# Kernel optimization log

Measured on AMD Instinct MI355X. Metric: run time of the kernel, lower is better.

## Reference

```python
import jax, jax.numpy as jnp
import numpy as np

WINDOW = 16  # hardcoded in module __init__

B, S, E, H = 2, 2048, 1024, 16
HD = E // H


def setup_inputs() -> dict:
    key = jax.random.key(0)
    k1, k2, k3, k4, k5, k6 = jax.random.split(key, 6)
    input_embeddings = jax.random.normal(k1, (B, S, E), dtype=jnp.float32)
    token_ids = jax.random.randint(k2, (B, S), 0, 32000, dtype=jnp.int64)
    # nn.MultiheadAttention parameters: packed in_proj (3E, E) + bias, out_proj (E, E) + bias
    in_proj_weight = jax.random.normal(k3, (3 * E, E), dtype=jnp.float32) * 0.02
    in_proj_bias = jax.random.normal(k4, (3 * E,), dtype=jnp.float32) * 0.02
    out_proj_weight = jax.random.normal(k5, (E, E), dtype=jnp.float32) * 0.02
    out_proj_bias = jax.random.normal(k6, (E,), dtype=jnp.float32) * 0.02
    return {
        "input_embeddings": input_embeddings,
        "token_ids": token_ids,
        "in_proj_weight": in_proj_weight,
        "in_proj_bias": in_proj_bias,
        "out_proj_weight": out_proj_weight,
        "out_proj_bias": out_proj_bias,
    }


def _blocked_mask(seq_len: int) -> jnp.ndarray:
    # Module sets mask[i, j] = True for j in [i - WINDOW, i] (17 positions).
    # PyTorch bool attn_mask: True = NOT allowed to attend.
    i = jnp.arange(seq_len)[:, None]
    j = jnp.arange(seq_len)[None, :]
    return (j <= i) & (j >= i - WINDOW)  # [S, S] bool, True = masked out


def reference(input_embeddings, token_ids, in_proj_weight, in_proj_bias,
              out_proj_weight, out_proj_bias):
    x = input_embeddings  # [B, S, E]
    b, s, e = x.shape
    # Packed QKV projection (torch Linear: y = x W^T + b)
    qkv = jnp.einsum('bse,fe->bsf', x, in_proj_weight) + in_proj_bias  # [B, S, 3E]
    q, k, v = jnp.split(qkv, 3, axis=-1)
    # Split heads: [B, H, S, HD]
    q = q.reshape(b, s, H, HD).transpose(0, 2, 1, 3)
    k = k.reshape(b, s, H, HD).transpose(0, 2, 1, 3)
    v = v.reshape(b, s, H, HD).transpose(0, 2, 1, 3)
    scale = 1.0 / jnp.sqrt(jnp.asarray(HD, dtype=x.dtype))
    scores = jnp.einsum('bhqd,bhkd->bhqk', q * scale, k)  # [B, H, S, S]
    blocked = _blocked_mask(s)  # True = masked
    scores = jnp.where(blocked[None, None, :, :], -jnp.inf, scores)
    attn = jax.nn.softmax(scores, axis=-1)
    ctx = jnp.einsum('bhqk,bhkd->bhqd', attn, v)  # [B, H, S, HD]
    ctx = ctx.transpose(0, 2, 1, 3).reshape(b, s, e)
    out = jnp.einsum('bse,fe->bsf', ctx, out_proj_weight) + out_proj_bias
    return out
```

## Files before the change

### kernel.cpp

```cpp
#include <hip/hip_runtime.h>

typedef __attribute__((ext_vector_type(8))) __bf16 bf16x8;
typedef __attribute__((ext_vector_type(4))) float f32x4;
typedef unsigned short u16;
typedef unsigned int u32;

#define MFMA16(a, b, c) __builtin_amdgcn_mfma_f32_16x16x32_bf16((a), (b), (c), 0, 0, 0)

__device__ __forceinline__ u16 f2bf(float f) {
  u32 u = __float_as_uint(f);
  return (u16)((u + 0x7fffu + ((u >> 16) & 1u)) >> 16);
}

#define BDIM 2
#define SDIM 2048
#define EDIM 1024
#define HDIM 16
#define HD 64
#define MDIM (BDIM * SDIM)

#define SC_C1 0.1803368801111355f
#define SC_C2 4.328085122667252e+01f

#define SW(r) ((((r) & 3) ^ (((r) >> 2) & 3)))

typedef __attribute__((address_space(3))) void lds_void;
typedef __attribute__((address_space(1))) void g_void;

__device__ __forceinline__ void async_lds16(const void* g, void* lds_byte) {
  __builtin_amdgcn_global_load_lds((const g_void*)g, (lds_void*)lds_byte, 16, 0, 0);
}

__global__ __launch_bounds__(256) void cvt_kernel(const float* __restrict__ src,
                                                  u16* __restrict__ dst, int n) {
  int i = (blockIdx.x * 256 + threadIdx.x) * 8;
  if (i >= n) return;
  float4 f0 = *(const float4*)(src + i);
  float4 f1 = *(const float4*)(src + i + 4);
  union { uint4 u; u16 s[8]; } o;
  o.s[0] = f2bf(f0.x); o.s[1] = f2bf(f0.y); o.s[2] = f2bf(f0.z); o.s[3] = f2bf(f0.w);
  o.s[4] = f2bf(f1.x); o.s[5] = f2bf(f1.y); o.s[6] = f2bf(f1.z); o.s[7] = f2bf(f1.w);
  *(uint4*)(dst + i) = o.u;
}

__global__ __launch_bounds__(256) void gemm_qkv_kernel(
    const u16* __restrict__ X, const u16* __restrict__ W,
    const float* __restrict__ bias, u16* __restrict__ qb,
    u16* __restrict__ kb, u16* __restrict__ vtb) {
  __shared__ __align__(16) u16 As[128 * 32];
  __shared__ __align__(16) u16 Bs[128 * 32];
  const int m0 = blockIdx.x * 128, n0 = blockIdx.y * 128;
  const int t = threadIdx.x;
  const int l = t & 63;
  const int quad = l >> 4, col = l & 15;
  const int wid = t >> 6;
  const int mh = wid & 1, nh = wid >> 1;
  const int wofs = (t & 192) << 4;
  f32x4 acc[4][4] = {};
  const u16* Ab = X + (size_t)m0 * EDIM;
  const u16* Bb = W + (size_t)n0 * EDIM;
  char* AsB = (char*)As;
  char* BsB = (char*)Bs;

  for (int k0 = 0; k0 < EDIM; k0 += 32) {
    __syncthreads();
#pragma unroll
    for (int p = 0; p < 2; p++) {
      int idx = p * 256 + t;
      int row = idx >> 2;
      int kq = (idx & 3) ^ SW(row);
      async_lds16(Ab + (size_t)row * EDIM + k0 + kq * 8, AsB + p * 4096 + wofs);
      async_lds16(Bb + (size_t)row * EDIM + k0 + kq * 8, BsB + p * 4096 + wofs);
    }
    __syncthreads();
    bf16x8 af[4], bfr[4];
#pragma unroll
    for (int i = 0; i < 4; i++) {
      int ra = 64 * mh + 16 * i + col;
      af[i] = *(const bf16x8*)&As[(ra * 4 + (quad ^ SW(ra))) * 8];
      int rb = 64 * nh + 16 * i + col;
      bfr[i] = *(const bf16x8*)&Bs[(rb * 4 + (quad ^ SW(rb))) * 8];
    }
#pragma unroll
    for (int i = 0; i < 4; i++)
#pragma unroll
      for (int j = 0; j < 4; j++)
        acc[i][j] = MFMA16(af[i], bfr[j], acc[i][j]);
  }

#pragma unroll
  for (int i = 0; i < 4; i++)
#pragma unroll
    for (int j = 0; j < 4; j++)
#pragma unroll
      for (int r = 0; r < 4; r++) {
        int m = m0 + 64 * mh + 16 * i + quad * 4 + r;
        int n = n0 + 64 * nh + 16 * j + col;
        float val = acc[i][j][r] + bias[n];
        int which = n >> 10, e = n & 1023;
        int hh = e >> 6, d = e & 63;
        int bb = m >> 11, s = m & 2047;
        u16 bv = f2bf(val);
        size_t hb = (size_t)(bb * HDIM + hh);
        if (which == 0)
          qb[(hb * SDIM + s) * HD + d] = bv;
        else if (which == 1)
          kb[(hb * SDIM + s) * HD + d] = bv;
        else
          vtb[(hb * HD + d) * SDIM + s] = bv;
      }
}

__global__ __launch_bounds__(256) void attn_kernel(
    const u16* __restrict__ qg, const u16* __restrict__ kg,
    const u16* __restrict__ vtg, u16* __restrict__ ctx) {
  __shared__ __align__(16) u16 Ks[64 * 64];
  __shared__ __align__(16) u16 Vs[64 * 64];
  __shared__ __align__(16) u16 Ps[64 * 68];

  const int bh = blockIdx.x;
  const int q0 = blockIdx.y * 64;
  const int t = threadIdx.x;
  const int wid = t >> 6, l = t & 63;
  const int quad = l >> 4, col = l & 15;
  const size_t base = (size_t)bh * SDIM * HD;

  bf16x8 aq[2];
  {
    const u16* qp = qg + base + (size_t)(q0 + 16 * wid + col) * HD + quad * 8;
    aq[0] = *(const bf16x8*)(qp);
    aq[1] = *(const bf16x8*)(qp + 32);
  }
  const int qrow = q0 + 16 * wid + quad * 4;

  const int srow = t >> 3;
  const int g = (t & 7) ^ (srow & 7);
  const u16* kptr = kg + base + (size_t)srow * HD + g * 8;
  const u16* vptr = vtg + base + (size_t)srow * SDIM + g * 8;
  char* ldsK = (char*)Ks + ((t & 192) << 4);
  char* ldsV = (char*)Vs + ((t & 192) << 4);

  float psum[4] = {0.f, 0.f, 0.f, 0.f};
  f32x4 oacc[4] = {};

  for (int kt = 0; kt < SDIM / 64; kt++) {
    const int k0 = kt * 64;
    __syncthreads();
    async_lds16(kptr + (size_t)k0 * HD, ldsK);
    async_lds16(kptr + (size_t)(k0 + 32) * HD, ldsK + 4096);
    async_lds16(vptr + k0, ldsV);
    async_lds16(vptr + (size_t)32 * SDIM + k0, ldsV + 4096);
    __syncthreads();

    f32x4 sc[4] = {};
#pragma unroll
    for (int half = 0; half < 2; half++)
#pragma unroll
      for (int ct = 0; ct < 4; ct++) {
        int r = 16 * ct + col;
        int phys = (4 * half + quad) ^ (r & 7);
        bf16x8 bfrag = *(const bf16x8*)&Ks[r * 64 + phys * 8];
        sc[ct] = MFMA16(aq[half], bfrag, sc[ct]);
      }

    const int pbase = (16 * wid + quad * 4) * 68 + col;
    if (k0 <= q0 + 63 && k0 + 63 >= q0 - 16) {
#pragma unroll
      for (int ct = 0; ct < 4; ct++)
#pragma unroll
        for (int r = 0; r < 4; r++) {
          int i = qrow + r, j = k0 + 16 * ct + col;
          float arg = sc[ct][r] * SC_C1 - SC_C2;
          arg = (j <= i && j + 16 >= i) ? -1.0e30f : arg;
          float p = __builtin_exp2f(arg);
          psum[r] += p;
          Ps[pbase + r * 68 + 16 * ct] = f2bf(p);
        }
    } else {
#pragma unroll
      for (int ct = 0; ct < 4; ct++)
#pragma unroll
        for (int r = 0; r < 4; r++) {
          float p = __builtin_exp2f(sc[ct][r] * SC_C1 - SC_C2);
          psum[r] += p;
          Ps[pbase + r * 68 + 16 * ct] = f2bf(p);
        }
    }

#pragma unroll
    for (int half = 0; half < 2; half++) {
      bf16x8 pa = *(const bf16x8*)&Ps[(16 * wid + col) * 68 + half * 32 + quad * 8];
#pragma unroll
      for (int dt = 0; dt < 4; dt++) {
        int vr = 16 * dt + col;
        int phys = (4 * half + quad) ^ (vr & 7);
        bf16x8 vbf = *(const bf16x8*)&Vs[vr * 64 + phys * 8];
        oacc[dt] = MFMA16(pa, vbf, oacc[dt]);
      }
    }
  }

#pragma unroll
  for (int off = 1; off < 16; off <<= 1)
#pragma unroll
    for (int r = 0; r < 4; r++) psum[r] += __shfl_xor(psum[r], off, 64);

  const int b = bh >> 4, h = bh & 15;
  float linv[4];
#pragma unroll
  for (int r = 0; r < 4; r++) linv[r] = 1.0f / psum[r];
#pragma unroll
  for (int dt = 0; dt < 4; dt++)
#pragma unroll
    for (int r = 0; r < 4; r++) {
      int qgl = qrow + r;
      int d = 16 * dt + col;
      ctx[((size_t)(b * SDIM + qgl)) * EDIM + h * HD + d] =
          f2bf(oacc[dt][r] * linv[r]);
    }
}

__global__ __launch_bounds__(256) void gemm_out_kernel(
    const u16* __restrict__ A, const u16* __restrict__ W,
    const float* __restrict__ bias, float* __restrict__ out) {
  __shared__ __align__(16) u16 As[128 * 32];
  __shared__ __align__(16) u16 Bs[128 * 32];
  const int m0 = blockIdx.x * 128, n0 = blockIdx.y * 128;
  const int t = threadIdx.x;
  const int l = t & 63;
  const int quad = l >> 4, col = l & 15;
  const int wid = t >> 6;
  const int mh = wid & 1, nh = wid >> 1;
  const int wofs = (t & 192) << 4;
  f32x4 acc[4][4] = {};
  const u16* Ab = A + (size_t)m0 * EDIM;
  const u16* Bb = W + (size_t)n0 * EDIM;
  char* AsB = (char*)As;
  char* BsB = (char*)Bs;

  for (int k0 = 0; k0 < EDIM; k0 += 32) {
    __syncthreads();
#pragma unroll
    for (int p = 0; p < 2; p++) {
      int idx = p * 256 + t;
      int row = idx >> 2;
      int kq = (idx & 3) ^ SW(row);
      async_lds16(Ab + (size_t)row * EDIM + k0 + kq * 8, AsB + p * 4096 + wofs);
      async_lds16(Bb + (size_t)row * EDIM + k0 + kq * 8, BsB + p * 4096 + wofs);
    }
    __syncthreads();
    bf16x8 af[4], bfr[4];
#pragma unroll
    for (int i = 0; i < 4; i++) {
      int ra = 64 * mh + 16 * i + col;
      af[i] = *(const bf16x8*)&As[(ra * 4 + (quad ^ SW(ra))) * 8];
      int rb = 64 * nh + 16 * i + col;
      bfr[i] = *(const bf16x8*)&Bs[(rb * 4 + (quad ^ SW(rb))) * 8];
    }
#pragma unroll
    for (int i = 0; i < 4; i++)
#pragma unroll
      for (int j = 0; j < 4; j++)
        acc[i][j] = MFMA16(af[i], bfr[j], acc[i][j]);
  }

#pragma unroll
  for (int i = 0; i < 4; i++)
#pragma unroll
    for (int j = 0; j < 4; j++)
#pragma unroll
      for (int r = 0; r < 4; r++) {
        int m = m0 + 64 * mh + 16 * i + quad * 4 + r;
        int n = n0 + 64 * nh + 16 * j + col;
        out[(size_t)m * EDIM + n] = acc[i][j][r] + bias[n];
      }
}

extern "C" void kernel_launch(void* const* d_in, const int* in_sizes, int n_in,
                              void* d_out, int out_size, void* d_ws,
                              size_t ws_size, hipStream_t stream) {
  const float* x = (const float*)d_in[0];
  const float* in_w = (const float*)d_in[2];
  const float* in_b = (const float*)d_in[3];
  const float* out_w = (const float*)d_in[4];
  const float* out_b = (const float*)d_in[5];
  float* out = (float*)d_out;

  char* ws = (char*)d_ws;
  u16* Xb  = (u16*)ws;
  u16* ctx = (u16*)ws;
  u16* qb  = (u16*)(ws + (size_t)( 8 << 20));
  u16* kb  = (u16*)(ws + (size_t)(16 << 20));
  u16* vtb = (u16*)(ws + (size_t)(24 << 20));
  u16* Wib = (u16*)(ws + (size_t)(32 << 20));
  u16* Wob = (u16*)(ws + (size_t)(38 << 20));

  cvt_kernel<<<2048, 256, 0, stream>>>(x, Xb, MDIM * EDIM);
  cvt_kernel<<<1536, 256, 0, stream>>>(in_w, Wib, 3 * EDIM * EDIM);
  cvt_kernel<<<512, 256, 0, stream>>>(out_w, Wob, EDIM * EDIM);

  gemm_qkv_kernel<<<dim3(MDIM / 128, 3 * EDIM / 128), 256, 0, stream>>>(
      Xb, Wib, in_b, qb, kb, vtb);
  attn_kernel<<<dim3(BDIM * HDIM, SDIM / 64), 256, 0, stream>>>(qb, kb, vtb, ctx);
  gemm_out_kernel<<<dim3(MDIM / 128, EDIM / 128), 256, 0, stream>>>(
      ctx, Wob, out_b, out);
}
```

Baseline: 241.0 us.

## Double attention query tile per block, transpose V GEMM tiles, simplify bf16 rounding

The attention kernel now gives each block 128 query rows (32 per wave, two 16-row subtiles), so every K/V tile loaded into LDS is reused by twice as many queries. This halves global K/V traffic and barrier count, at the cost of more registers and half as many blocks. The QKV GEMM swaps MFMA operands for the V blocks so that the transposed V stores become contiguous along the sequence dimension. The bf16 conversion drops round-to-nearest-even for a plain round-half-up, which saves a few ALU ops but can change rounding on ties.

```diff
diff --git a/kernel.cpp b/kernel.cpp
--- a/kernel.cpp
+++ b/kernel.cpp
@@ -8,8 +8,7 @@
 #define MFMA16(a, b, c) __builtin_amdgcn_mfma_f32_16x16x32_bf16((a), (b), (c), 0, 0, 0)
 
 __device__ __forceinline__ u16 f2bf(float f) {
-  u32 u = __float_as_uint(f);
-  return (u16)((u + 0x7fffu + ((u >> 16) & 1u)) >> 16);
+  return (u16)((__float_as_uint(f) + 0x8000u) >> 16);
 }
 
 #define BDIM 2
@@ -50,6 +49,7 @@
   __shared__ __align__(16) u16 As[128 * 32];
   __shared__ __align__(16) u16 Bs[128 * 32];
   const int m0 = blockIdx.x * 128, n0 = blockIdx.y * 128;
+  const bool isV = (n0 >= 2 * EDIM);
   const int t = threadIdx.x;
   const int l = t & 63;
   const int quad = l >> 4, col = l & 15;
@@ -81,34 +81,53 @@
       int rb = 64 * nh + 16 * i + col;
       bfr[i] = *(const bf16x8*)&Bs[(rb * 4 + (quad ^ SW(rb))) * 8];
     }
+    if (isV) {
+#pragma unroll
+      for (int i = 0; i < 4; i++)
+#pragma unroll
+        for (int j = 0; j < 4; j++)
+          acc[i][j] = MFMA16(bfr[i], af[j], acc[i][j]);
+    } else {
+#pragma unroll
+      for (int i = 0; i < 4; i++)
+#pragma unroll
+        for (int j = 0; j < 4; j++)
+          acc[i][j] = MFMA16(af[i], bfr[j], acc[i][j]);
+    }
+  }
+
+  if (isV) {
 #pragma unroll
     for (int i = 0; i < 4; i++)
 #pragma unroll
       for (int j = 0; j < 4; j++)
-        acc[i][j] = MFMA16(af[i], bfr[j], acc[i][j]);
-  }
-
-#pragma unroll
-  for (int i = 0; i < 4; i++)
-#pragma unroll
-    for (int j = 0; j < 4; j++)
-#pragma unroll
-      for (int r = 0; r < 4; r++) {
-        int m = m0 + 64 * mh + 16 * i + quad * 4 + r;
-        int n = n0 + 64 * nh + 16 * j + col;
-        float val = acc[i][j][r] + bias[n];
-        int which = n >> 10, e = n & 1023;
-        int hh = e >> 6, d = e & 63;
-        int bb = m >> 11, s = m & 2047;
-        u16 bv = f2bf(val);
-        size_t hb = (size_t)(bb * HDIM + hh);
-        if (which == 0)
-          qb[(hb * SDIM + s) * HD + d] = bv;
-        else if (which == 1)
-          kb[(hb * SDIM + s) * HD + d] = bv;
-        else
-          vtb[(hb * HD + d) * SDIM + s] = bv;
-      }
+#pragma unroll
+        for (int r = 0; r < 4; r++) {
+          int n = n0 + 64 * nh + 16 * i + quad * 4 + r;
+          int m = m0 + 64 * mh + 16 * j + col;
+          float val = acc[i][j][r] + bias[n];
+          int e = n & 1023;
+          int hh = e >> 6, d = e & 63;
+          int bb = m >> 11, s = m & 2047;
+          vtb[(((size_t)(bb * HDIM + hh)) * HD + d) * SDIM + s] = f2bf(val);
+        }
+  } else {
+#pragma unroll
+    for (int i = 0; i < 4; i++)
+#pragma unroll
+      for (int j = 0; j < 4; j++)
+#pragma unroll
+        for (int r = 0; r < 4; r++) {
+          int m = m0 + 64 * mh + 16 * i + quad * 4 + r;
+          int n = n0 + 64 * nh + 16 * j + col;
+          float val = acc[i][j][r] + bias[n];
+          int which = n >> 10, e = n & 1023;
+          int hh = e >> 6, d = e & 63;
+          int bb = m >> 11, s = m & 2047;
+          u16* dst = (which == 0) ? qb : kb;
+          dst[(((size_t)(bb * HDIM + hh)) * SDIM + s) * HD + d] = f2bf(val);
+        }
+  }
 }
 
 __global__ __launch_bounds__(256) void attn_kernel(
@@ -116,22 +135,24 @@
     const u16* __restrict__ vtg, u16* __restrict__ ctx) {
   __shared__ __align__(16) u16 Ks[64 * 64];
   __shared__ __align__(16) u16 Vs[64 * 64];
-  __shared__ __align__(16) u16 Ps[64 * 68];
+  __shared__ __align__(16) u16 Ps[128 * 68];
 
   const int bh = blockIdx.x;
-  const int q0 = blockIdx.y * 64;
+  const int q0 = blockIdx.y * 128;
   const int t = threadIdx.x;
   const int wid = t >> 6, l = t & 63;
   const int quad = l >> 4, col = l & 15;
   const size_t base = (size_t)bh * SDIM * HD;
 
-  bf16x8 aq[2];
-  {
-    const u16* qp = qg + base + (size_t)(q0 + 16 * wid + col) * HD + quad * 8;
-    aq[0] = *(const bf16x8*)(qp);
-    aq[1] = *(const bf16x8*)(qp + 32);
-  }
-  const int qrow = q0 + 16 * wid + quad * 4;
+  bf16x8 aq[2][2];
+#pragma unroll
+  for (int sub = 0; sub < 2; sub++) {
+    const u16* qp =
+        qg + base + (size_t)(q0 + 32 * wid + 16 * sub + col) * HD + quad * 8;
+    aq[sub][0] = *(const bf16x8*)(qp);
+    aq[sub][1] = *(const bf16x8*)(qp + 32);
+  }
+  const int qrow0 = q0 + 32 * wid + quad * 4;
 
   const int srow = t >> 3;
   const int g = (t & 7) ^ (srow & 7);
@@ -140,8 +161,8 @@
   char* ldsK = (char*)Ks + ((t & 192) << 4);
   char* ldsV = (char*)Vs + ((t & 192) << 4);
 
-  float psum[4] = {0.f, 0.f, 0.f, 0.f};
-  f32x4 oacc[4] = {};
+  float psum[2][4] = {};
+  f32x4 oacc[2][4] = {};
 
   for (int kt = 0; kt < SDIM / 64; kt++) {
     const int k0 = kt * 64;
@@ -152,7 +173,7 @@
     async_lds16(vptr + (size_t)32 * SDIM + k0, ldsV + 4096);
     __syncthreads();
 
-    f32x4 sc[4] = {};
+    f32x4 sc[2][4] = {};
 #pragma unroll
     for (int half = 0; half < 2; half++)
 #pragma unroll
@@ -160,42 +181,51 @@
         int r = 16 * ct + col;
         int phys = (4 * half + quad) ^ (r & 7);
         bf16x8 bfrag = *(const bf16x8*)&Ks[r * 64 + phys * 8];
-        sc[ct] = MFMA16(aq[half], bfrag, sc[ct]);
-      }
-
-    const int pbase = (16 * wid + quad * 4) * 68 + col;
-    if (k0 <= q0 + 63 && k0 + 63 >= q0 - 16) {
-#pragma unroll
-      for (int ct = 0; ct < 4; ct++)
-#pragma unroll
-        for (int r = 0; r < 4; r++) {
-          int i = qrow + r, j = k0 + 16 * ct + col;
-          float arg = sc[ct][r] * SC_C1 - SC_C2;
-          arg = (j <= i && j + 16 >= i) ? -1.0e30f : arg;
-          float p = __builtin_exp2f(arg);
-          psum[r] += p;
-          Ps[pbase + r * 68 + 16 * ct] = f2bf(p);
-        }
-    } else {
-#pragma unroll
-      for (int ct = 0; ct < 4; ct++)
-#pragma unroll
-        for (int r = 0; r < 4; r++) {
-          float p = __builtin_exp2f(sc[ct][r] * SC_C1 - SC_C2);
-          psum[r] += p;
-          Ps[pbase + r * 68 + 16 * ct] = f2bf(p);
-        }
+        sc[0][ct] = MFMA16(aq[0][half], bfrag, sc[0][ct]);
+        sc[1][ct] = MFMA16(aq[1][half], bfrag, sc[1][ct]);
+      }
+
+    const bool maskt = (k0 <= q0 + 127) && (k0 + 63 >= q0 - 16);
+#pragma unroll
+    for (int sub = 0; sub < 2; sub++) {
+      const int pbase = (32 * wid + 16 * sub + quad * 4) * 68 + col;
+      if (maskt) {
+#pragma unroll
+        for (int ct = 0; ct < 4; ct++)
+#pragma unroll
+          for (int r = 0; r < 4; r++) {
+            int i = qrow0 + 16 * sub + r, j = k0 + 16 * ct + col;
+            float arg = sc[sub][ct][r] * SC_C1 - SC_C2;
+            arg = (j <= i && j + 16 >= i) ? -1.0e30f : arg;
+            float p = __builtin_exp2f(arg);
+            psum[sub][r] += p;
+            Ps[pbase + r * 68 + 16 * ct] = f2bf(p);
+          }
+      } else {
+#pragma unroll
+        for (int ct = 0; ct < 4; ct++)
+#pragma unroll
+          for (int r = 0; r < 4; r++) {
+            float p = __builtin_exp2f(sc[sub][ct][r] * SC_C1 - SC_C2);
+            psum[sub][r] += p;
+            Ps[pbase + r * 68 + 16 * ct] = f2bf(p);
+          }
+      }
     }
 
 #pragma unroll
     for (int half = 0; half < 2; half++) {
-      bf16x8 pa = *(const bf16x8*)&Ps[(16 * wid + col) * 68 + half * 32 + quad * 8];
+      bf16x8 pa0 =
+          *(const bf16x8*)&Ps[(32 * wid + col) * 68 + half * 32 + quad * 8];
+      bf16x8 pa1 =
+          *(const bf16x8*)&Ps[(32 * wid + 16 + col) * 68 + half * 32 + quad * 8];
 #pragma unroll
       for (int dt = 0; dt < 4; dt++) {
         int vr = 16 * dt + col;
         int phys = (4 * half + quad) ^ (vr & 7);
         bf16x8 vbf = *(const bf16x8*)&Vs[vr * 64 + phys * 8];
-        oacc[dt] = MFMA16(pa, vbf, oacc[dt]);
+        oacc[0][dt] = MFMA16(pa0, vbf, oacc[0][dt]);
+        oacc[1][dt] = MFMA16(pa1, vbf, oacc[1][dt]);
       }
     }
   }
@@ -203,21 +233,27 @@
 #pragma unroll
   for (int off = 1; off < 16; off <<= 1)
 #pragma unroll
-    for (int r = 0; r < 4; r++) psum[r] += __shfl_xor(psum[r], off, 64);
+    for (int sub = 0; sub < 2; sub++)
+#pragma unroll
+      for (int r = 0; r < 4; r++)
+        psum[sub][r] += __shfl_xor(psum[sub][r], off, 64);
 
   const int b = bh >> 4, h = bh & 15;
-  float linv[4];
-#pragma unroll
-  for (int r = 0; r < 4; r++) linv[r] = 1.0f / psum[r];
-#pragma unroll
-  for (int dt = 0; dt < 4; dt++)
-#pragma unroll
-    for (int r = 0; r < 4; r++) {
-      int qgl = qrow + r;
-      int d = 16 * dt + col;
-      ctx[((size_t)(b * SDIM + qgl)) * EDIM + h * HD + d] =
-          f2bf(oacc[dt][r] * linv[r]);
-    }
+#pragma unroll
+  for (int sub = 0; sub < 2; sub++) {
+    float linv[4];
+#pragma unroll
+    for (int r = 0; r < 4; r++) linv[r] = 1.0f / psum[sub][r];
+#pragma unroll
+    for (int dt = 0; dt < 4; dt++)
+#pragma unroll
+      for (int r = 0; r < 4; r++) {
+        int qgl = qrow0 + 16 * sub + r;
+        int d = 16 * dt + col;
+        ctx[((size_t)(b * SDIM + qgl)) * EDIM + h * HD + d] =
+            f2bf(oacc[sub][dt][r] * linv[r]);
+      }
+  }
 }
 
 __global__ __launch_bounds__(256) void gemm_out_kernel(
@@ -301,7 +337,7 @@
 
   gemm_qkv_kernel<<<dim3(MDIM / 128, 3 * EDIM / 128), 256, 0, stream>>>(
       Xb, Wib, in_b, qb, kb, vtb);
-  attn_kernel<<<dim3(BDIM * HDIM, SDIM / 64), 256, 0, stream>>>(qb, kb, vtb, ctx);
+  attn_kernel<<<dim3(BDIM * HDIM, SDIM / 128), 256, 0, stream>>>(qb, kb, vtb, ctx);
   gemm_out_kernel<<<dim3(MDIM / 128, EDIM / 128), 256, 0, stream>>>(
       ctx, Wob, out_b, out);
 }
```

Result: faster. 225.9 us (-6.3%).
